# Kernel optimization log

Hardware: AMD Instinct MI355X
Metric: run time of the kernel (lower is better)

The kernel has to match this reference:

```python
import jax, jax.numpy as jnp
import numpy as np

EMBED_DIM = 384


def setup_inputs() -> dict:
    key = jax.random.key(0)
    k1, k2, k3 = jax.random.split(key, 3)
    B, P, N, C = 32, 4, 1024, EMBED_DIM
    x = jax.random.normal(k1, (B, P, N, C), dtype=jnp.float32)
    # 1x1 Conv2D on channel-last == linear on last dim; kernel [Cin, Cout]
    w_qkv = jax.random.normal(k2, (C, 1 + 2 * C), dtype=jnp.float32) * (1.0 / np.sqrt(C))
    b_qkv = jnp.zeros((1 + 2 * C,), dtype=jnp.float32)
    w_proj = jax.random.normal(k3, (C, C), dtype=jnp.float32) * (1.0 / np.sqrt(C))
    b_proj = jnp.zeros((C,), dtype=jnp.float32)
    return {"x": x, "w_qkv": w_qkv, "b_qkv": b_qkv, "w_proj": w_proj, "b_proj": b_proj}


def reference(x, w_qkv, b_qkv, w_proj, b_proj):
    C = EMBED_DIM
    # qkv pointwise conv: [B,P,N,C] @ [C, 1+2C]
    qkv = jnp.einsum('bpnc,cd->bpnd', x, w_qkv) + b_qkv
    query = qkv[..., :1]                 # [B,P,N,1]
    key_t = qkv[..., 1:1 + C]            # [B,P,N,C]
    value = qkv[..., 1 + C:]             # [B,P,N,C]
    # NOTE: softmax over the trailing axis of size 1 (faithful to source) -> all ones
    context_scores = jax.nn.softmax(query, axis=-1)
    # key * scores, reduce-sum over patch-index axis (axis=2), keepdims
    context_vector = jnp.sum(key_t * context_scores, axis=2, keepdims=True)  # [B,P,1,C]
    gated = jax.nn.relu(value) * context_vector                              # [B,P,N,C]
    out = jnp.einsum('bpnc,cd->bpnd', gated, w_proj) + b_proj
    return out
```

## Files before the change

### kernel.cpp

```cpp
#include <hip/hip_runtime.h>
#include <hip/hip_bf16.h>
#include <type_traits>
#include <utility>

#define C_     384
#define N_     1024
#define G_     128
#define QKVD   769
#define TILE_B 24576

typedef float  f32x4 __attribute__((ext_vector_type(4)));
typedef short  s16x8 __attribute__((ext_vector_type(8)));
typedef __bf16 b16x8 __attribute__((ext_vector_type(8)));

template <typename V, typename = void>
struct mfma_takes : std::false_type {};
template <typename V>
struct mfma_takes<V, std::void_t<decltype(__builtin_amdgcn_mfma_f32_16x16x32_bf16(
    std::declval<V>(), std::declval<V>(), std::declval<f32x4>(), 0, 0, 0))>>
    : std::true_type {};

using frag_t = std::conditional_t<mfma_takes<s16x8>::value, s16x8, b16x8>;

template <typename V>
__device__ __forceinline__ f32x4 mfma_bf16(V a, V b, f32x4 c) {
  return __builtin_amdgcn_mfma_f32_16x16x32_bf16(a, b, c, 0, 0, 0);
}

__device__ __forceinline__ unsigned short f2bf(float f) {
  union { float f; unsigned u; } v; v.f = f;
  unsigned r = v.u + 0x7fffu + ((v.u >> 16) & 1u);
  return (unsigned short)(r >> 16);
}
__device__ __forceinline__ unsigned pack2(float lo, float hi) {
  return (unsigned)f2bf(lo) | ((unsigned)f2bf(hi) << 16);
}

__device__ __forceinline__ void stage16(const char* g, char* lbase, int lane) {
#if __has_builtin(__builtin_amdgcn_global_load_lds)
  __builtin_amdgcn_global_load_lds(
      (const __attribute__((address_space(1))) void*)g,
      (__attribute__((address_space(3))) void*)lbase, 16, 0, 0);
#else
  *(uint4*)(lbase + lane * 16) = *(const uint4*)g;
#endif
}

__global__ __launch_bounds__(384) void k_prep(const float* __restrict__ x,
                                              char* __restrict__ xbb,
                                              float* __restrict__ xsum) {
  __shared__ float csum[C_];
  const int b    = blockIdx.x;
  const int g    = b >> 4;
  const int tid  = threadIdx.x;
  const int col8 = (tid % 48) * 8;
  const int rg   = tid / 48;
  csum[tid] = 0.f;
  __syncthreads();

  const float* xg = x + ((size_t)b * 64 + (size_t)rg * 8) * C_ + col8;
  char* img = xbb + (size_t)b * 2 * TILE_B;
  float s0=0,s1=0,s2=0,s3=0,s4=0,s5=0,s6=0,s7=0;
#pragma unroll
  for (int j = 0; j < 8; ++j) {
    int row = rg * 8 + j;
    float4 a = *(const float4*)(xg + (size_t)j * C_);
    float4 c = *(const float4*)(xg + (size_t)j * C_ + 4);
    uint4 w;
    w.x = pack2(a.x, a.y); w.y = pack2(a.z, a.w);
    w.z = pack2(c.x, c.y); w.w = pack2(c.z, c.w);
    int rt = row & 31;
    int tl = row >> 5;
    *(uint4*)(img + tl * TILE_B + ((rt * 768 + col8 * 2) ^ ((rt & 7) << 4))) = w;
    s0 += a.x; s1 += a.y; s2 += a.z; s3 += a.w;
    s4 += c.x; s5 += c.y; s6 += c.z; s7 += c.w;
  }
  atomicAdd(&csum[col8 + 0], s0); atomicAdd(&csum[col8 + 1], s1);
  atomicAdd(&csum[col8 + 2], s2); atomicAdd(&csum[col8 + 3], s3);
  atomicAdd(&csum[col8 + 4], s4); atomicAdd(&csum[col8 + 5], s5);
  atomicAdd(&csum[col8 + 6], s6); atomicAdd(&csum[col8 + 7], s7);
  __syncthreads();
  atomicAdd(&xsum[g * C_ + tid], csum[tid]);
}

__global__ __launch_bounds__(384) void k_xsum(const float* __restrict__ x,
                                              float* __restrict__ xsum) {
  __shared__ float sh[4][C_];
  const int tid = threadIdx.x;
  const int c4  = (tid % 96) * 4;
  const int rg  = tid / 96;
  const int b   = blockIdx.x;
  const int g   = b >> 3;
  const float* p = x + ((size_t)b * 128 + (size_t)rg * 32) * C_ + c4;
  f32x4 s = {0.f, 0.f, 0.f, 0.f};
#pragma unroll 8
  for (int r = 0; r < 32; ++r) {
    float4 v = *(const float4*)(p + (size_t)r * C_);
    s.x += v.x; s.y += v.y; s.z += v.z; s.w += v.w;
  }
  *(f32x4*)&sh[rg][c4] = s;
  __syncthreads();
  if (rg == 0) {
#pragma unroll
    for (int j = 0; j < 4; ++j) {
      float v = sh[0][c4 + j] + sh[1][c4 + j] + sh[2][c4 + j] + sh[3][c4 + j];
      atomicAdd(&xsum[g * C_ + c4 + j], v);
    }
  }
}

__global__ void k_cv(const float* __restrict__ xsum, const float* __restrict__ w_qkv,
                     const float* __restrict__ b_qkv, float* __restrict__ cv) {
  __shared__ float xs[C_];
  int g = blockIdx.x, c = threadIdx.x;
  xs[c] = xsum[g * C_ + c];
  __syncthreads();
  float acc = 0.f;
#pragma unroll 4
  for (int k = 0; k < C_; ++k) acc += xs[k] * w_qkv[k * QKVD + 1 + c];
  cv[g * C_ + c] = acc + (float)N_ * b_qkv[1 + c];
}

__global__ void k_pack(const float* __restrict__ w_qkv, const float* __restrict__ w_proj,
                       unsigned short* __restrict__ pWv, unsigned short* __restrict__ pWp) {
  int bid = blockIdx.x;
  int mat = bid / 288;
  int r   = bid % 288;
  int kk = r / 24, nf = r % 24;
  int lane = threadIdx.x;
  int kbase = kk * 32 + (lane >> 4) * 8;
  int n = nf * 16 + (lane & 15);
  unsigned v[4];
#pragma unroll
  for (int jj = 0; jj < 4; ++jj) {
    int k0 = kbase + jj * 2;
    float f0 = mat ? w_proj[(size_t)k0 * C_ + n]       : w_qkv[(size_t)k0 * QKVD + 385 + n];
    float f1 = mat ? w_proj[(size_t)(k0 + 1) * C_ + n] : w_qkv[(size_t)(k0 + 1) * QKVD + 385 + n];
    v[jj] = (unsigned)f2bf(f0) | ((unsigned)f2bf(f1) << 16);
  }
  unsigned short* dst = (mat ? pWp : pWv) + ((size_t)r * 64 + lane) * 8;
  uint4 w; w.x = v[0]; w.y = v[1]; w.z = v[2]; w.w = v[3];
  *(uint4*)dst = w;
}

template <bool PRE>
__global__ __launch_bounds__(512) void k_fused(
    const float* __restrict__ x, const char* __restrict__ xbb,
    const unsigned short* __restrict__ pWv, const unsigned short* __restrict__ pWp,
    const float* __restrict__ cv, const float* __restrict__ b_qkv,
    const float* __restrict__ b_proj, float* __restrict__ out) {
  __shared__ __align__(16) char tile[32 * 768];
  __shared__ float cv_l[C_], bv_l[C_], bp_l[C_];

  const int tid  = threadIdx.x;
  const int lane = tid & 63;
  const int wv   = tid >> 6;
  const int R0   = blockIdx.x * 32;
  const int g    = R0 >> 10;

  if (tid < C_) {
    cv_l[tid] = cv[g * C_ + tid];
    bv_l[tid] = b_qkv[1 + C_ + tid];
    bp_l[tid] = b_proj[tid];
  }

  if constexpr (PRE) {
    const char* img = xbb + (size_t)blockIdx.x * TILE_B;
#pragma unroll
    for (int j = 0; j < 3; ++j) {
      int cb = (wv * 3 + j) * 1024;
      stage16(img + cb + lane * 16, tile + cb, lane);
    }
  } else {
    const float* xg = x + (size_t)R0 * C_;
#pragma unroll
    for (int j = 0; j < 3; ++j) {
      int ch  = tid + j * 512;
      int row = ch / 48;
      int c8  = (ch % 48) * 8;
      const float4* s0 = (const float4*)(xg + (size_t)row * C_ + c8);
      float4 a = s0[0], b = s0[1];
      uint4 w;
      w.x = pack2(a.x, a.y); w.y = pack2(a.z, a.w);
      w.z = pack2(b.x, b.y); w.w = pack2(b.z, b.w);
      int byte = (row * 768 + c8 * 2) ^ ((row & 7) << 4);
      *(uint4*)(tile + byte) = w;
    }
  }
  __syncthreads();

  const f32x4 zero = {0.f, 0.f, 0.f, 0.f};
  f32x4 acc[2][3];
#pragma unroll
  for (int m = 0; m < 2; ++m)
#pragma unroll
    for (int n = 0; n < 3; ++n) acc[m][n] = zero;

  for (int kk = 0; kk < 12; ++kk) {
    frag_t A[2], Bv[3];
    int kb2 = (kk * 32 + (lane >> 4) * 8) * 2;
#pragma unroll
    for (int m = 0; m < 2; ++m) {
      int row = m * 16 + (lane & 15);
      A[m] = *(const frag_t*)(tile + ((row * 768 + kb2) ^ ((row & 7) << 4)));
    }
    const unsigned short* bp_ = pWv + ((size_t)(kk * 24 + wv * 3) * 64 + lane) * 8;
#pragma unroll
    for (int n = 0; n < 3; ++n) Bv[n] = *(const frag_t*)(bp_ + (size_t)n * 64 * 8);
#pragma unroll
    for (int m = 0; m < 2; ++m)
#pragma unroll
      for (int n = 0; n < 3; ++n) acc[m][n] = mfma_bf16(A[m], Bv[n], acc[m][n]);
  }
  __syncthreads();

#pragma unroll
  for (int m = 0; m < 2; ++m) {
#pragma unroll
    for (int n = 0; n < 3; ++n) {
      int col = wv * 48 + n * 16 + (lane & 15);
      float cvv = cv_l[col], bvv = bv_l[col];
#pragma unroll
      for (int r = 0; r < 4; ++r) {
        int row = m * 16 + (lane >> 4) * 4 + r;
        float val = fmaxf(acc[m][n][r] + bvv, 0.f) * cvv;
        *(unsigned short*)(tile + ((row * 768 + col * 2) ^ ((row & 7) << 4))) = f2bf(val);
      }
    }
  }
  __syncthreads();

#pragma unroll
  for (int m = 0; m < 2; ++m)
#pragma unroll
    for (int n = 0; n < 3; ++n) acc[m][n] = zero;

  for (int kk = 0; kk < 12; ++kk) {
    frag_t A[2], Bv[3];
    int kb2 = (kk * 32 + (lane >> 4) * 8) * 2;
#pragma unroll
    for (int m = 0; m < 2; ++m) {
      int row = m * 16 + (lane & 15);
      A[m] = *(const frag_t*)(tile + ((row * 768 + kb2) ^ ((row & 7) << 4)));
    }
    const unsigned short* bp_ = pWp + ((size_t)(kk * 24 + wv * 3) * 64 + lane) * 8;
#pragma unroll
    for (int n = 0; n < 3; ++n) Bv[n] = *(const frag_t*)(bp_ + (size_t)n * 64 * 8);
#pragma unroll
    for (int m = 0; m < 2; ++m)
#pragma unroll
      for (int n = 0; n < 3; ++n) acc[m][n] = mfma_bf16(A[m], Bv[n], acc[m][n]);
  }

#pragma unroll
  for (int m = 0; m < 2; ++m) {
#pragma unroll
    for (int n = 0; n < 3; ++n) {
      int col = wv * 48 + n * 16 + (lane & 15);
      float bpv = bp_l[col];
#pragma unroll
      for (int r = 0; r < 4; ++r) {
        int row = m * 16 + (lane >> 4) * 4 + r;
        out[(size_t)(R0 + row) * C_ + col] = acc[m][n][r] + bpv;
      }
    }
  }
}

extern "C" void kernel_launch(void* const* d_in, const int* in_sizes, int n_in,
                              void* d_out, int out_size, void* d_ws, size_t ws_size,
                              hipStream_t stream) {
  const float* x      = (const float*)d_in[0];
  const float* w_qkv  = (const float*)d_in[1];
  const float* b_qkv  = (const float*)d_in[2];
  const float* w_proj = (const float*)d_in[3];
  const float* b_proj = (const float*)d_in[4];
  float* out = (float*)d_out;

  float* xsum = (float*)d_ws;
  float* cvp  = xsum + G_ * C_;
  unsigned short* pWv = (unsigned short*)(cvp + G_ * C_);
  unsigned short* pWp = pWv + C_ * C_;
  char* xbb = (char*)(pWp + C_ * C_);

  const size_t need = 983040 + (size_t)4096 * TILE_B;

  hipMemsetAsync(xsum, 0, G_ * C_ * sizeof(float), stream);
  k_pack<<<576, 64, 0, stream>>>(w_qkv, w_proj, pWv, pWp);

  if (ws_size >= need) {
    k_prep<<<2048, 384, 0, stream>>>(x, xbb, xsum);
    k_cv<<<G_, C_, 0, stream>>>(xsum, w_qkv, b_qkv, cvp);
    k_fused<true><<<4096, 512, 0, stream>>>(x, xbb, pWv, pWp, cvp, b_qkv, b_proj, out);
  } else {
    k_xsum<<<1024, 384, 0, stream>>>(x, xsum);
    k_cv<<<G_, C_, 0, stream>>>(xsum, w_qkv, b_qkv, cvp);
    k_fused<false><<<4096, 512, 0, stream>>>(x, xbb, pWv, pWp, cvp, b_qkv, b_proj, out);
  }
}
```

Before: 233.1 us.

## Fold weight packing into prep kernel and enlarge per-block prep work

```diff
diff --git a/kernel.cpp b/kernel.cpp
--- a/kernel.cpp
+++ b/kernel.cpp
@@ -46,41 +46,70 @@
 #endif
 }
 
-__global__ __launch_bounds__(384) void k_prep(const float* __restrict__ x,
-                                              char* __restrict__ xbb,
-                                              float* __restrict__ xsum) {
-  __shared__ float csum[C_];
-  const int b    = blockIdx.x;
-  const int g    = b >> 4;
-  const int tid  = threadIdx.x;
-  const int col8 = (tid % 48) * 8;
-  const int rg   = tid / 48;
-  csum[tid] = 0.f;
-  __syncthreads();
-
-  const float* xg = x + ((size_t)b * 64 + (size_t)rg * 8) * C_ + col8;
-  char* img = xbb + (size_t)b * 2 * TILE_B;
-  float s0=0,s1=0,s2=0,s3=0,s4=0,s5=0,s6=0,s7=0;
-#pragma unroll
-  for (int j = 0; j < 8; ++j) {
-    int row = rg * 8 + j;
-    float4 a = *(const float4*)(xg + (size_t)j * C_);
-    float4 c = *(const float4*)(xg + (size_t)j * C_ + 4);
-    uint4 w;
-    w.x = pack2(a.x, a.y); w.y = pack2(a.z, a.w);
-    w.z = pack2(c.x, c.y); w.w = pack2(c.z, c.w);
-    int rt = row & 31;
-    int tl = row >> 5;
-    *(uint4*)(img + tl * TILE_B + ((rt * 768 + col8 * 2) ^ ((rt & 7) << 4))) = w;
-    s0 += a.x; s1 += a.y; s2 += a.z; s3 += a.w;
-    s4 += c.x; s5 += c.y; s6 += c.z; s7 += c.w;
-  }
-  atomicAdd(&csum[col8 + 0], s0); atomicAdd(&csum[col8 + 1], s1);
-  atomicAdd(&csum[col8 + 2], s2); atomicAdd(&csum[col8 + 3], s3);
-  atomicAdd(&csum[col8 + 4], s4); atomicAdd(&csum[col8 + 5], s5);
-  atomicAdd(&csum[col8 + 6], s6); atomicAdd(&csum[col8 + 7], s7);
-  __syncthreads();
-  atomicAdd(&xsum[g * C_ + tid], csum[tid]);
+__global__ __launch_bounds__(512) void k_prep(
+    const float* __restrict__ x, const float* __restrict__ w_qkv,
+    const float* __restrict__ w_proj, char* __restrict__ xbb,
+    float* __restrict__ xsum, unsigned short* __restrict__ pWv,
+    unsigned short* __restrict__ pWp) {
+  const int b   = blockIdx.x;
+  const int tid = threadIdx.x;
+
+  if (b < 512) {
+    __shared__ float csum[C_];
+    const int g = b >> 2;
+    for (int c = tid; c < C_; c += 512) csum[c] = 0.f;
+    __syncthreads();
+
+    if (tid < 384) {
+      const int col8 = (tid % 48) * 8;
+      const int rg   = tid / 48;
+      const float* xg = x + (size_t)b * 256 * C_ + col8;
+      char* img = xbb + (size_t)b * 8 * TILE_B;
+      float s0=0,s1=0,s2=0,s3=0,s4=0,s5=0,s6=0,s7=0;
+#pragma unroll 1
+      for (int im = 0; im < 8; ++im) {
+#pragma unroll
+        for (int j = 0; j < 4; ++j) {
+          int row = rg * 4 + j;
+          const float* src = xg + ((size_t)im * 32 + row) * C_;
+          float4 a = *(const float4*)(src);
+          float4 c = *(const float4*)(src + 4);
+          uint4 w;
+          w.x = pack2(a.x, a.y); w.y = pack2(a.z, a.w);
+          w.z = pack2(c.x, c.y); w.w = pack2(c.z, c.w);
+          *(uint4*)(img + im * TILE_B +
+                    ((row * 768 + col8 * 2) ^ ((row & 7) << 4))) = w;
+          s0 += a.x; s1 += a.y; s2 += a.z; s3 += a.w;
+          s4 += c.x; s5 += c.y; s6 += c.z; s7 += c.w;
+        }
+      }
+      atomicAdd(&csum[col8 + 0], s0); atomicAdd(&csum[col8 + 1], s1);
+      atomicAdd(&csum[col8 + 2], s2); atomicAdd(&csum[col8 + 3], s3);
+      atomicAdd(&csum[col8 + 4], s4); atomicAdd(&csum[col8 + 5], s5);
+      atomicAdd(&csum[col8 + 6], s6); atomicAdd(&csum[col8 + 7], s7);
+    }
+    __syncthreads();
+    if (tid < 384) atomicAdd(&xsum[g * C_ + tid], csum[tid]);
+  } else {
+    int pb   = (b - 512) * 8 + (tid >> 6);
+    int mat  = pb / 288;
+    int r    = pb % 288;
+    int kk   = r / 24, nf = r % 24;
+    int lane = tid & 63;
+    int kbase = kk * 32 + (lane >> 4) * 8;
+    int n     = nf * 16 + (lane & 15);
+    unsigned v[4];
+#pragma unroll
+    for (int jj = 0; jj < 4; ++jj) {
+      int k0 = kbase + jj * 2;
+      float f0 = mat ? w_proj[(size_t)k0 * C_ + n]       : w_qkv[(size_t)k0 * QKVD + 385 + n];
+      float f1 = mat ? w_proj[(size_t)(k0 + 1) * C_ + n] : w_qkv[(size_t)(k0 + 1) * QKVD + 385 + n];
+      v[jj] = (unsigned)f2bf(f0) | ((unsigned)f2bf(f1) << 16);
+    }
+    unsigned short* dst = (mat ? pWp : pWv) + ((size_t)r * 64 + lane) * 8;
+    uint4 w; w.x = v[0]; w.y = v[1]; w.z = v[2]; w.w = v[3];
+    *(uint4*)dst = w;
+  }
 }
 
 __global__ __launch_bounds__(384) void k_xsum(const float* __restrict__ x,
@@ -109,18 +138,6 @@
   }
 }
 
-__global__ void k_cv(const float* __restrict__ xsum, const float* __restrict__ w_qkv,
-                     const float* __restrict__ b_qkv, float* __restrict__ cv) {
-  __shared__ float xs[C_];
-  int g = blockIdx.x, c = threadIdx.x;
-  xs[c] = xsum[g * C_ + c];
-  __syncthreads();
-  float acc = 0.f;
-#pragma unroll 4
-  for (int k = 0; k < C_; ++k) acc += xs[k] * w_qkv[k * QKVD + 1 + c];
-  cv[g * C_ + c] = acc + (float)N_ * b_qkv[1 + c];
-}
-
 __global__ void k_pack(const float* __restrict__ w_qkv, const float* __restrict__ w_proj,
                        unsigned short* __restrict__ pWv, unsigned short* __restrict__ pWp) {
   int bid = blockIdx.x;
@@ -141,6 +158,18 @@
   unsigned short* dst = (mat ? pWp : pWv) + ((size_t)r * 64 + lane) * 8;
   uint4 w; w.x = v[0]; w.y = v[1]; w.z = v[2]; w.w = v[3];
   *(uint4*)dst = w;
+}
+
+__global__ void k_cv(const float* __restrict__ xsum, const float* __restrict__ w_qkv,
+                     const float* __restrict__ b_qkv, float* __restrict__ cv) {
+  __shared__ float xs[C_];
+  int g = blockIdx.x, c = threadIdx.x;
+  xs[c] = xsum[g * C_ + c];
+  __syncthreads();
+  float acc = 0.f;
+#pragma unroll 4
+  for (int k = 0; k < C_; ++k) acc += xs[k] * w_qkv[k * QKVD + 1 + c];
+  cv[g * C_ + c] = acc + (float)N_ * b_qkv[1 + c];
 }
 
 template <bool PRE>
@@ -286,13 +315,13 @@
   const size_t need = 983040 + (size_t)4096 * TILE_B;
 
   hipMemsetAsync(xsum, 0, G_ * C_ * sizeof(float), stream);
-  k_pack<<<576, 64, 0, stream>>>(w_qkv, w_proj, pWv, pWp);
 
   if (ws_size >= need) {
-    k_prep<<<2048, 384, 0, stream>>>(x, xbb, xsum);
+    k_prep<<<584, 512, 0, stream>>>(x, w_qkv, w_proj, xbb, xsum, pWv, pWp);
     k_cv<<<G_, C_, 0, stream>>>(xsum, w_qkv, b_qkv, cvp);
     k_fused<true><<<4096, 512, 0, stream>>>(x, xbb, pWv, pWp, cvp, b_qkv, b_proj, out);
   } else {
+    k_pack<<<576, 64, 0, stream>>>(w_qkv, w_proj, pWv, pWp);
     k_xsum<<<1024, 384, 0, stream>>>(x, xsum);
     k_cv<<<G_, C_, 0, stream>>>(xsum, w_qkv, b_qkv, cvp);
     k_fused<false><<<4096, 512, 0, stream>>>(x, xbb, pWv, pWp, cvp, b_qkv, b_proj, out);
```

After: 239.8 us. +2.9%, slower.
